# Kernel tuning notes

Hardware: AMD Instinct MI355X
Metric: run time of the kernel (lower is better)

Reference implementation:

```python
import jax, jax.numpy as jnp
import numpy as np

B, L, H, E = 4, 2048, 8, 64

def setup_inputs() -> dict:
    key = jax.random.key(0)
    kq, kk, kv = jax.random.split(key, 3)
    queries = jax.random.normal(kq, (B, L, H, E), dtype=jnp.float32)
    keys = jax.random.normal(kk, (B, L, H, E), dtype=jnp.float32)
    values = jax.random.normal(kv, (B, L, H, E), dtype=jnp.float32)
    return {"queries": queries, "keys": keys, "values": values}

def reference(queries, keys, values):
    # queries/keys/values: [B, L, H, E]
    E_ = queries.shape[-1]
    scale = 1.0 / jnp.sqrt(jnp.float32(E_))
    # scores: [B, H, L, S]
    scores = jnp.einsum('blhe,bshe->bhls', queries, keys)
    Lq, S = scores.shape[-2], scores.shape[-1]
    # TriangularCausalMask: mask positions where s > l (strict upper triangle)
    causal = jnp.tril(jnp.ones((Lq, S), dtype=bool))
    scores = jnp.where(causal, scores, -jnp.inf)
    A = jax.nn.softmax(scale * scores, axis=-1)  # dropout p=0 -> identity
    V = jnp.einsum('bhls,bshd->blhd', A, values)
    return V
```

## Files before the change

kernel.cpp:

```cpp
#include <hip/hip_runtime.h>


#define Bc 4
#define Lc 2048
#define Hc 8
#define Ec 64
#define TILEB 8192
#define NKV 32
#define BHB ((size_t)NKV * TILEB)
#define WSV ((size_t)32 * BHB)

using f32x4 = __attribute__((ext_vector_type(4))) float;
using f16x8 = __attribute__((ext_vector_type(8))) _Float16;
using f16x4 = __attribute__((ext_vector_type(4))) _Float16;
using hf16x2 = __fp16 __attribute__((ext_vector_type(2)));
using u32x4 = __attribute__((ext_vector_type(4))) unsigned int;

static __device__ __forceinline__ unsigned int pk2(float lo, float hi) {
    union { hf16x2 h; unsigned int u; } c;
    c.h = __builtin_amdgcn_cvt_pkrtz(lo, hi);
    return c.u;
}
static __device__ __forceinline__ u32x4 nt16(const void* p) {
    return __builtin_nontemporal_load((const u32x4*)p);
}

__global__ __launch_bounds__(256)
void prep_kernel(const float* __restrict__ K, const float* __restrict__ V,
                 char* __restrict__ ws)
{
    __shared__ char kst[64 * 128];
    __shared__ char vst[64 * 144];
    __shared__ char vtt[64 * 128];

    const int bid = blockIdx.x;
    const int bh = bid >> 5, kt = bid & 31;
    const int b = bh >> 3, h = bh & 7;
    const int tid = threadIdx.x;
    const size_t base = (size_t)b * Lc * Hc * Ec + (size_t)h * Ec;

    {
        const int r = tid >> 2, q4 = tid & 3, c0 = 16 * q4;
        const float* kp = K + base + (size_t)(kt * 64 + r) * 512 + c0;
        const float* vp = V + base + (size_t)(kt * 64 + r) * 512 + c0;
        unsigned int wk[8], wv[8];
        #pragma unroll
        for (int i = 0; i < 4; ++i) {
            union { u32x4 v; float f[4]; } fk, fv;
            fk.v = nt16(kp + 4 * i);
            fv.v = nt16(vp + 4 * i);
            wk[2*i]   = pk2(fk.f[0], fk.f[1]); wk[2*i+1] = pk2(fk.f[2], fk.f[3]);
            wv[2*i]   = pk2(fv.f[0], fv.f[1]); wv[2*i+1] = pk2(fv.f[2], fv.f[3]);
        }
        *(uint4*)(kst + r * 128 + 2 * c0)      = *(uint4*)&wk[0];
        *(uint4*)(kst + r * 128 + 2 * c0 + 16) = *(uint4*)&wk[4];
        *(uint4*)(vst + r * 144 + 2 * c0)      = *(uint4*)&wv[0];
        *(uint4*)(vst + r * 144 + 2 * c0 + 16) = *(uint4*)&wv[4];
    }
    __syncthreads();
    {
        const int e = tid >> 2, kq = tid & 3, kv0 = 16 * kq;
        unsigned int w[8];
        #pragma unroll
        for (int i = 0; i < 8; ++i) {
            unsigned int lo = *(const unsigned short*)(vst + (kv0 + 2*i)     * 144 + 2*e);
            unsigned int hi = *(const unsigned short*)(vst + (kv0 + 2*i + 1) * 144 + 2*e);
            w[i] = lo | (hi << 16);
        }
        *(uint4*)(vtt + e * 128 + 2 * kv0)      = *(uint4*)&w[0];
        *(uint4*)(vtt + e * 128 + 2 * kv0 + 16) = *(uint4*)&w[4];
    }
    __syncthreads();
    {
        const int lane = tid & 63, qq = tid >> 6;
        const int l15 = lane & 15, l4 = lane >> 4;
        char* ko = ws + (size_t)bh * BHB + (size_t)kt * TILEB;
        char* vo = ws + WSV + (size_t)bh * BHB + (size_t)kt * TILEB;
        uint4 k0 = *(const uint4*)(kst + (16 * qq + l15) * 128 + 16 * l4);
        uint4 k1 = *(const uint4*)(kst + (16 * qq + l15) * 128 + 64 + 16 * l4);
        *(uint4*)(ko + (2 * qq)     * 1024 + lane * 16) = k0;
        *(uint4*)(ko + (2 * qq + 1) * 1024 + lane * 16) = k1;
        unsigned long long vv[4];
        #pragma unroll
        for (int c = 0; c < 4; ++c)
            vv[c] = *(const unsigned long long*)(vtt + (16 * c + l15) * 128 + 32 * qq + 8 * l4);
        uint4 v01, v23;
        v01.x = (unsigned)vv[0]; v01.y = (unsigned)(vv[0] >> 32);
        v01.z = (unsigned)vv[1]; v01.w = (unsigned)(vv[1] >> 32);
        v23.x = (unsigned)vv[2]; v23.y = (unsigned)(vv[2] >> 32);
        v23.z = (unsigned)vv[3]; v23.w = (unsigned)(vv[3] >> 32);
        *(uint4*)(vo + (2 * qq)     * 1024 + lane * 16) = v01;
        *(uint4*)(vo + (2 * qq + 1) * 1024 + lane * 16) = v23;
    }
}

__global__ __launch_bounds__(256, 3)
void fa_fwd_kernel(const float* __restrict__ Q, const char* __restrict__ ws,
                   float* __restrict__ Out)
{
    const int bid = blockIdx.x;
    const int qi  = bid >> 5;
    const int bh  = bid & 31;
    const int qt  = 31 - qi;
    const int b   = bh >> 3, h = bh & 7;

    const int tid  = threadIdx.x;
    const int wid  = tid >> 6;
    const int lane = tid & 63;
    const int l15  = lane & 15, l4 = lane >> 4;

    const size_t base = (size_t)b * Lc * Hc * Ec + (size_t)h * Ec;
    const char* kimg = ws + (size_t)bh * BHB + lane * 16;
    const char* vimg = ws + WSV + (size_t)bh * BHB + lane * 16;
    const float SL2E = 0.125f * 1.44269504088896340736f;

    const int qrow0 = qt * 64 + 16 * wid;
    const int mysteps = qt + 1;

    f16x8 qa0, qa1;
    {
        const float* qpr = Q + base + (size_t)(qrow0 + l15) * 512 + 8 * l4;
        union { u32x4 v; float f[4]; } f0, f1, f2, f3;
        f0.v = nt16(qpr);      f1.v = nt16(qpr + 4);
        f2.v = nt16(qpr + 32); f3.v = nt16(qpr + 36);
        union { f16x8 v; unsigned int u[4]; } pk;
        pk.u[0] = pk2(f0.f[0] * SL2E, f0.f[1] * SL2E);
        pk.u[1] = pk2(f0.f[2] * SL2E, f0.f[3] * SL2E);
        pk.u[2] = pk2(f1.f[0] * SL2E, f1.f[1] * SL2E);
        pk.u[3] = pk2(f1.f[2] * SL2E, f1.f[3] * SL2E);
        qa0 = pk.v;
        pk.u[0] = pk2(f2.f[0] * SL2E, f2.f[1] * SL2E);
        pk.u[1] = pk2(f2.f[2] * SL2E, f2.f[3] * SL2E);
        pk.u[2] = pk2(f3.f[0] * SL2E, f3.f[1] * SL2E);
        pk.u[3] = pk2(f3.f[2] * SL2E, f3.f[3] * SL2E);
        qa1 = pk.v;
    }

    f32x4 o[4] = {};
    float lsum = 0.f;
    float m_run = 8.0f;

    uint4 kf[8], vf[8];
    #pragma unroll
    for (int j = 0; j < 8; ++j) kf[j] = *(const uint4*)(kimg + j * 1024);
    #pragma unroll
    for (int j = 0; j < 8; ++j) vf[j] = *(const uint4*)(vimg + j * 1024);

    #pragma unroll 1
    for (int kt = 0; kt < mysteps; ++kt) {
        const int nxt = (kt + 1 < mysteps) ? kt + 1 : kt;
        const char* kp = kimg + (size_t)nxt * TILEB;
        const char* vp = vimg + (size_t)nxt * TILEB;
        const bool last = (kt == mysteps - 1);

        #pragma unroll
        for (int m = 0; m < 4; ++m) {
            union { uint4 u; f16x8 h; } a0, a1;
            a0.u = kf[2 * m]; a1.u = kf[2 * m + 1];
            f32x4 s = {0.f, 0.f, 0.f, 0.f};
            s = __builtin_amdgcn_mfma_f32_16x16x32_f16(a0.h, qa0, s, 0, 0, 0);
            s = __builtin_amdgcn_mfma_f32_16x16x32_f16(a1.h, qa1, s, 0, 0, 0);

            kf[2 * m]     = *(const uint4*)(kp + (2 * m)     * 1024);
            kf[2 * m + 1] = *(const uint4*)(kp + (2 * m + 1) * 1024);

            if (last) {
                const int q_g = qrow0 + l15;
                #pragma unroll
                for (int r2 = 0; r2 < 4; ++r2) {
                    const int kv_g = kt * 64 + 16 * m + 4 * l4 + r2;
                    if (kv_g > q_g) s[r2] = -1e30f;
                }
            }

            const float cmax = fmaxf(fmaxf(s[0], s[1]), fmaxf(s[2], s[3]));
            if (__any(cmax > m_run)) {
                float pm = cmax;
                pm = fmaxf(pm, __shfl_xor(pm, 16, 64));
                pm = fmaxf(pm, __shfl_xor(pm, 32, 64));
                const float m_new = fmaxf(m_run, pm);
                const float fac = __builtin_exp2f(m_run - m_new);
                m_run = m_new;
                lsum *= fac;
                float fr[4];
                #pragma unroll
                for (int r2 = 0; r2 < 4; ++r2) fr[r2] = __shfl(fac, 4 * l4 + r2, 64);
                #pragma unroll
                for (int c = 0; c < 4; ++c)
                    #pragma unroll
                    for (int r2 = 0; r2 < 4; ++r2) o[c][r2] *= fr[r2];
            }

            const float p0 = __builtin_exp2f(s[0] - m_run);
            const float p1 = __builtin_exp2f(s[1] - m_run);
            const float p2 = __builtin_exp2f(s[2] - m_run);
            const float p3 = __builtin_exp2f(s[3] - m_run);
            lsum += (p0 + p1) + (p2 + p3);
            union { f16x4 h; unsigned int u[2]; } pa;
            pa.u[0] = pk2(p0, p1);
            pa.u[1] = pk2(p2, p3);

            union { uint4 u; f16x4 h[2]; } w0, w1;
            w0.u = vf[2 * m]; w1.u = vf[2 * m + 1];
            o[0] = __builtin_amdgcn_mfma_f32_16x16x16f16(pa.h, w0.h[0], o[0], 0, 0, 0);
            o[1] = __builtin_amdgcn_mfma_f32_16x16x16f16(pa.h, w0.h[1], o[1], 0, 0, 0);
            o[2] = __builtin_amdgcn_mfma_f32_16x16x16f16(pa.h, w1.h[0], o[2], 0, 0, 0);
            o[3] = __builtin_amdgcn_mfma_f32_16x16x16f16(pa.h, w1.h[1], o[3], 0, 0, 0);

            vf[2 * m]     = *(const uint4*)(vp + (2 * m)     * 1024);
            vf[2 * m + 1] = *(const uint4*)(vp + (2 * m + 1) * 1024);
        }
    }

    lsum += __shfl_xor(lsum, 16, 64);
    lsum += __shfl_xor(lsum, 32, 64);
    const float inv = 1.0f / lsum;
    float ir[4];
    #pragma unroll
    for (int r2 = 0; r2 < 4; ++r2) ir[r2] = __shfl(inv, 4 * l4 + r2, 64);
    float* op = Out + base;
    #pragma unroll
    for (int c = 0; c < 4; ++c)
        #pragma unroll
        for (int r2 = 0; r2 < 4; ++r2)
            __builtin_nontemporal_store(o[c][r2] * ir[r2],
                op + (size_t)(qrow0 + 4 * l4 + r2) * 512 + 16 * c + l15);
}

extern "C" void kernel_launch(void* const* d_in, const int* in_sizes, int n_in,
                              void* d_out, int out_size, void* d_ws, size_t ws_size,
                              hipStream_t stream) {
    const float* Q = (const float*)d_in[0];
    const float* K = (const float*)d_in[1];
    const float* V = (const float*)d_in[2];
    float* O = (float*)d_out;
    char* ws = (char*)d_ws;
    hipLaunchKernelGGL(prep_kernel, dim3(32 * NKV), dim3(256), 0, stream, K, V, ws);
    hipLaunchKernelGGL(fa_fwd_kernel, dim3(32 * 32), dim3(256), 0, stream, Q, ws, O);
}
```

Before: 67.83 us.

## Process two 16-row query groups per wave to reuse K/V fragments

Each wave now handles 32 query rows (two MFMA groups) and each block handles 128 query rows instead of 64, so every K/V fragment loaded from the workspace feeds two sets of MFMAs. The grid is halved and the q-tile order is changed to a zig-zag over the 16 tiles, with per-wave step counts adjusted for the causal boundary. Occupancy is lowered to 2 blocks per CU because of the extra registers for the doubled accumulators. Waves within a block now have different step counts, and the output stores switch from nontemporal to plain stores.

```diff
diff --git a/kernel.cpp b/kernel.cpp
--- a/kernel.cpp
+++ b/kernel.cpp
@@ -94,14 +94,14 @@
     }
 }
 
-__global__ __launch_bounds__(256, 3)
+__global__ __launch_bounds__(256, 2)
 void fa_fwd_kernel(const float* __restrict__ Q, const char* __restrict__ ws,
                    float* __restrict__ Out)
 {
     const int bid = blockIdx.x;
     const int qi  = bid >> 5;
     const int bh  = bid & 31;
-    const int qt  = 31 - qi;
+    const int qt  = (qi < 8) ? (15 - qi) : (qi - 8);
     const int b   = bh >> 3, h = bh & 7;
 
     const int tid  = threadIdx.x;
@@ -114,12 +114,13 @@
     const char* vimg = ws + WSV + (size_t)bh * BHB + lane * 16;
     const float SL2E = 0.125f * 1.44269504088896340736f;
 
-    const int qrow0 = qt * 64 + 16 * wid;
-    const int mysteps = qt + 1;
-
-    f16x8 qa0, qa1;
-    {
-        const float* qpr = Q + base + (size_t)(qrow0 + l15) * 512 + 8 * l4;
+    const int qrow0 = qt * 128 + 32 * wid;
+    const int mysteps = 2 * qt + 1 + (wid >> 1);
+
+    f16x8 qa[2][2];
+    #pragma unroll
+    for (int g = 0; g < 2; ++g) {
+        const float* qpr = Q + base + (size_t)(qrow0 + 16 * g + l15) * 512 + 8 * l4;
         union { u32x4 v; float f[4]; } f0, f1, f2, f3;
         f0.v = nt16(qpr);      f1.v = nt16(qpr + 4);
         f2.v = nt16(qpr + 32); f3.v = nt16(qpr + 36);
@@ -128,17 +129,17 @@
         pk.u[1] = pk2(f0.f[2] * SL2E, f0.f[3] * SL2E);
         pk.u[2] = pk2(f1.f[0] * SL2E, f1.f[1] * SL2E);
         pk.u[3] = pk2(f1.f[2] * SL2E, f1.f[3] * SL2E);
-        qa0 = pk.v;
+        qa[g][0] = pk.v;
         pk.u[0] = pk2(f2.f[0] * SL2E, f2.f[1] * SL2E);
         pk.u[1] = pk2(f2.f[2] * SL2E, f2.f[3] * SL2E);
         pk.u[2] = pk2(f3.f[0] * SL2E, f3.f[1] * SL2E);
         pk.u[3] = pk2(f3.f[2] * SL2E, f3.f[3] * SL2E);
-        qa1 = pk.v;
-    }
-
-    f32x4 o[4] = {};
-    float lsum = 0.f;
-    float m_run = 8.0f;
+        qa[g][1] = pk.v;
+    }
+
+    f32x4 o[2][4] = {};
+    float lsum[2] = {0.f, 0.f};
+    float m_run[2] = {8.0f, 8.0f};
 
     uint4 kf[8], vf[8];
     #pragma unroll
@@ -148,83 +149,97 @@
 
     #pragma unroll 1
     for (int kt = 0; kt < mysteps; ++kt) {
-        const int nxt = (kt + 1 < mysteps) ? kt + 1 : kt;
-        const char* kp = kimg + (size_t)nxt * TILEB;
-        const char* vp = vimg + (size_t)nxt * TILEB;
         const bool last = (kt == mysteps - 1);
+        const char* kp = kimg + (size_t)(last ? 0 : kt + 1) * TILEB;
+        const char* vp = vimg + (size_t)(last ? 0 : kt + 1) * TILEB;
+        const int kv0 = kt * 64;
 
         #pragma unroll
         for (int m = 0; m < 4; ++m) {
             union { uint4 u; f16x8 h; } a0, a1;
             a0.u = kf[2 * m]; a1.u = kf[2 * m + 1];
-            f32x4 s = {0.f, 0.f, 0.f, 0.f};
-            s = __builtin_amdgcn_mfma_f32_16x16x32_f16(a0.h, qa0, s, 0, 0, 0);
-            s = __builtin_amdgcn_mfma_f32_16x16x32_f16(a1.h, qa1, s, 0, 0, 0);
+            f32x4 s[2];
+            #pragma unroll
+            for (int g = 0; g < 2; ++g) {
+                f32x4 z = {0.f, 0.f, 0.f, 0.f};
+                z = __builtin_amdgcn_mfma_f32_16x16x32_f16(a0.h, qa[g][0], z, 0, 0, 0);
+                z = __builtin_amdgcn_mfma_f32_16x16x32_f16(a1.h, qa[g][1], z, 0, 0, 0);
+                s[g] = z;
+            }
 
             kf[2 * m]     = *(const uint4*)(kp + (2 * m)     * 1024);
             kf[2 * m + 1] = *(const uint4*)(kp + (2 * m + 1) * 1024);
 
             if (last) {
-                const int q_g = qrow0 + l15;
                 #pragma unroll
-                for (int r2 = 0; r2 < 4; ++r2) {
-                    const int kv_g = kt * 64 + 16 * m + 4 * l4 + r2;
-                    if (kv_g > q_g) s[r2] = -1e30f;
+                for (int g = 0; g < 2; ++g) {
+                    const int q_g = qrow0 + 16 * g + l15;
+                    #pragma unroll
+                    for (int r2 = 0; r2 < 4; ++r2) {
+                        const int kv_g = kv0 + 16 * m + 4 * l4 + r2;
+                        if (kv_g > q_g) s[g][r2] = -1e30f;
+                    }
                 }
             }
 
-            const float cmax = fmaxf(fmaxf(s[0], s[1]), fmaxf(s[2], s[3]));
-            if (__any(cmax > m_run)) {
-                float pm = cmax;
-                pm = fmaxf(pm, __shfl_xor(pm, 16, 64));
-                pm = fmaxf(pm, __shfl_xor(pm, 32, 64));
-                const float m_new = fmaxf(m_run, pm);
-                const float fac = __builtin_exp2f(m_run - m_new);
-                m_run = m_new;
-                lsum *= fac;
-                float fr[4];
-                #pragma unroll
-                for (int r2 = 0; r2 < 4; ++r2) fr[r2] = __shfl(fac, 4 * l4 + r2, 64);
-                #pragma unroll
-                for (int c = 0; c < 4; ++c)
-                    #pragma unroll
-                    for (int r2 = 0; r2 < 4; ++r2) o[c][r2] *= fr[r2];
-            }
-
-            const float p0 = __builtin_exp2f(s[0] - m_run);
-            const float p1 = __builtin_exp2f(s[1] - m_run);
-            const float p2 = __builtin_exp2f(s[2] - m_run);
-            const float p3 = __builtin_exp2f(s[3] - m_run);
-            lsum += (p0 + p1) + (p2 + p3);
-            union { f16x4 h; unsigned int u[2]; } pa;
-            pa.u[0] = pk2(p0, p1);
-            pa.u[1] = pk2(p2, p3);
-
             union { uint4 u; f16x4 h[2]; } w0, w1;
             w0.u = vf[2 * m]; w1.u = vf[2 * m + 1];
-            o[0] = __builtin_amdgcn_mfma_f32_16x16x16f16(pa.h, w0.h[0], o[0], 0, 0, 0);
-            o[1] = __builtin_amdgcn_mfma_f32_16x16x16f16(pa.h, w0.h[1], o[1], 0, 0, 0);
-            o[2] = __builtin_amdgcn_mfma_f32_16x16x16f16(pa.h, w1.h[0], o[2], 0, 0, 0);
-            o[3] = __builtin_amdgcn_mfma_f32_16x16x16f16(pa.h, w1.h[1], o[3], 0, 0, 0);
+            #pragma unroll
+            for (int g = 0; g < 2; ++g) {
+                const float cmax = fmaxf(fmaxf(s[g][0], s[g][1]),
+                                         fmaxf(s[g][2], s[g][3]));
+                if (__any(cmax > m_run[g])) {
+                    float pm = cmax;
+                    pm = fmaxf(pm, __shfl_xor(pm, 16, 64));
+                    pm = fmaxf(pm, __shfl_xor(pm, 32, 64));
+                    const float m_new = fmaxf(m_run[g], pm);
+                    const float fac = __builtin_exp2f(m_run[g] - m_new);
+                    m_run[g] = m_new;
+                    lsum[g] *= fac;
+                    float fr[4];
+                    #pragma unroll
+                    for (int r2 = 0; r2 < 4; ++r2) fr[r2] = __shfl(fac, 4 * l4 + r2, 64);
+                    #pragma unroll
+                    for (int c = 0; c < 4; ++c)
+                        #pragma unroll
+                        for (int r2 = 0; r2 < 4; ++r2) o[g][c][r2] *= fr[r2];
+                }
+                const float p0 = __builtin_exp2f(s[g][0] - m_run[g]);
+                const float p1 = __builtin_exp2f(s[g][1] - m_run[g]);
+                const float p2 = __builtin_exp2f(s[g][2] - m_run[g]);
+                const float p3 = __builtin_exp2f(s[g][3] - m_run[g]);
+                lsum[g] += (p0 + p1) + (p2 + p3);
+                union { f16x4 h; unsigned int u[2]; } pa;
+                pa.u[0] = pk2(p0, p1);
+                pa.u[1] = pk2(p2, p3);
+                o[g][0] = __builtin_amdgcn_mfma_f32_16x16x16f16(pa.h, w0.h[0], o[g][0], 0, 0, 0);
+                o[g][1] = __builtin_amdgcn_mfma_f32_16x16x16f16(pa.h, w0.h[1], o[g][1], 0, 0, 0);
+                o[g][2] = __builtin_amdgcn_mfma_f32_16x16x16f16(pa.h, w1.h[0], o[g][2], 0, 0, 0);
+                o[g][3] = __builtin_amdgcn_mfma_f32_16x16x16f16(pa.h, w1.h[1], o[g][3], 0, 0, 0);
+            }
 
             vf[2 * m]     = *(const uint4*)(vp + (2 * m)     * 1024);
             vf[2 * m + 1] = *(const uint4*)(vp + (2 * m + 1) * 1024);
         }
     }
 
-    lsum += __shfl_xor(lsum, 16, 64);
-    lsum += __shfl_xor(lsum, 32, 64);
-    const float inv = 1.0f / lsum;
-    float ir[4];
-    #pragma unroll
-    for (int r2 = 0; r2 < 4; ++r2) ir[r2] = __shfl(inv, 4 * l4 + r2, 64);
     float* op = Out + base;
     #pragma unroll
-    for (int c = 0; c < 4; ++c)
-        #pragma unroll
-        for (int r2 = 0; r2 < 4; ++r2)
-            __builtin_nontemporal_store(o[c][r2] * ir[r2],
-                op + (size_t)(qrow0 + 4 * l4 + r2) * 512 + 16 * c + l15);
+    for (int g = 0; g < 2; ++g) {
+        float ls = lsum[g];
+        ls += __shfl_xor(ls, 16, 64);
+        ls += __shfl_xor(ls, 32, 64);
+        const float inv = 1.0f / ls;
+        float ir[4];
+        #pragma unroll
+        for (int r2 = 0; r2 < 4; ++r2) ir[r2] = __shfl(inv, 4 * l4 + r2, 64);
+        const int qr = qrow0 + 16 * g;
+        #pragma unroll
+        for (int c = 0; c < 4; ++c)
+            #pragma unroll
+            for (int r2 = 0; r2 < 4; ++r2)
+                op[(size_t)(qr + 4 * l4 + r2) * 512 + 16 * c + l15] = o[g][c][r2] * ir[r2];
+    }
 }
 
 extern "C" void kernel_launch(void* const* d_in, const int* in_sizes, int n_in,
@@ -236,5 +251,5 @@
     float* O = (float*)d_out;
     char* ws = (char*)d_ws;
     hipLaunchKernelGGL(prep_kernel, dim3(32 * NKV), dim3(256), 0, stream, K, V, ws);
-    hipLaunchKernelGGL(fa_fwd_kernel, dim3(32 * 32), dim3(256), 0, stream, Q, ws, O);
-}
+    hipLaunchKernelGGL(fa_fwd_kernel, dim3(16 * 32), dim3(256), 0, stream, Q, ws, O);
+}
```

New measurement: 69.37 us. 1.02x slower.

## Split long causal query tiles across two KV-halves with a merge kernel

Applied to the files above, without the earlier changes.

The 16 longest query tiles per head now have their KV loop split into two halves run by separate blocks. Each half writes unnormalized output, row sum and running max to a workspace slot, and a new merge kernel combines them with log-sum-exp weights. This balances the triangular causal workload and shortens the critical path of the longest blocks. Launch bounds also rise to 4 blocks per CU. The cost is an extra kernel launch and the partial-result traffic through the workspace, and the path falls back to the old kernel if the workspace is too small.

```diff
diff --git a/kernel.cpp b/kernel.cpp
--- a/kernel.cpp
+++ b/kernel.cpp
@@ -9,6 +9,8 @@
 #define NKV 32
 #define BHB ((size_t)NKV * TILEB)
 #define WSV ((size_t)32 * BHB)
+#define WSP ((size_t)64 * BHB)
+#define SLOT 17408
 
 using f32x4 = __attribute__((ext_vector_type(4))) float;
 using f16x8 = __attribute__((ext_vector_type(8))) _Float16;
@@ -94,15 +96,35 @@
     }
 }
 
-__global__ __launch_bounds__(256, 3)
-void fa_fwd_kernel(const float* __restrict__ Q, const char* __restrict__ ws,
+template<bool SPLIT>
+__global__ __launch_bounds__(256, 4)
+void fa_fwd_kernel(const float* __restrict__ Q, char* __restrict__ ws,
                    float* __restrict__ Out)
 {
     const int bid = blockIdx.x;
-    const int qi  = bid >> 5;
-    const int bh  = bid & 31;
-    const int qt  = 31 - qi;
-    const int b   = bh >> 3, h = bh & 7;
+    int qt, bh, kt0, kt1;
+    bool wpart = false;
+    char* slotp = nullptr;
+    if (SPLIT) {
+        if (bid < 1024) {
+            const int sq = bid >> 6; qt = 31 - sq;
+            const int rem = bid & 63;
+            const int half = rem >> 5; bh = rem & 31;
+            const int n0 = (qt + 2) >> 1;
+            kt0 = half ? n0 : 0;
+            kt1 = half ? (qt + 1) : n0;
+            wpart = true;
+            slotp = ws + WSP + (size_t)((sq << 6) + (bh << 1) + half) * SLOT;
+        } else {
+            const int u = bid - 1024;
+            qt = 15 - (u >> 5); bh = u & 31;
+            kt0 = 0; kt1 = qt + 1;
+        }
+    } else {
+        qt = 31 - (bid >> 5); bh = bid & 31;
+        kt0 = 0; kt1 = qt + 1;
+    }
+    const int b = bh >> 3, h = bh & 7;
 
     const int tid  = threadIdx.x;
     const int wid  = tid >> 6;
@@ -115,11 +137,11 @@
     const float SL2E = 0.125f * 1.44269504088896340736f;
 
     const int qrow0 = qt * 64 + 16 * wid;
-    const int mysteps = qt + 1;
+    const int q_g = qrow0 + l15;
 
     f16x8 qa0, qa1;
     {
-        const float* qpr = Q + base + (size_t)(qrow0 + l15) * 512 + 8 * l4;
+        const float* qpr = Q + base + (size_t)q_g * 512 + 8 * l4;
         union { u32x4 v; float f[4]; } f0, f1, f2, f3;
         f0.v = nt16(qpr);      f1.v = nt16(qpr + 4);
         f2.v = nt16(qpr + 32); f3.v = nt16(qpr + 36);
@@ -142,16 +164,16 @@
 
     uint4 kf[8], vf[8];
     #pragma unroll
-    for (int j = 0; j < 8; ++j) kf[j] = *(const uint4*)(kimg + j * 1024);
+    for (int j = 0; j < 8; ++j) kf[j] = *(const uint4*)(kimg + (size_t)kt0 * TILEB + j * 1024);
     #pragma unroll
-    for (int j = 0; j < 8; ++j) vf[j] = *(const uint4*)(vimg + j * 1024);
+    for (int j = 0; j < 8; ++j) vf[j] = *(const uint4*)(vimg + (size_t)kt0 * TILEB + j * 1024);
 
     #pragma unroll 1
-    for (int kt = 0; kt < mysteps; ++kt) {
-        const int nxt = (kt + 1 < mysteps) ? kt + 1 : kt;
+    for (int kt = kt0; kt < kt1; ++kt) {
+        const bool last = (kt == qt);
+        const int nxt = (kt + 1 < kt1) ? kt + 1 : kt0;
         const char* kp = kimg + (size_t)nxt * TILEB;
         const char* vp = vimg + (size_t)nxt * TILEB;
-        const bool last = (kt == mysteps - 1);
 
         #pragma unroll
         for (int m = 0; m < 4; ++m) {
@@ -165,7 +187,6 @@
             kf[2 * m + 1] = *(const uint4*)(kp + (2 * m + 1) * 1024);
 
             if (last) {
-                const int q_g = qrow0 + l15;
                 #pragma unroll
                 for (int r2 = 0; r2 < 4; ++r2) {
                     const int kv_g = kt * 64 + 16 * m + 4 * l4 + r2;
@@ -214,17 +235,70 @@
 
     lsum += __shfl_xor(lsum, 16, 64);
     lsum += __shfl_xor(lsum, 32, 64);
-    const float inv = 1.0f / lsum;
-    float ir[4];
+
+    if (SPLIT && wpart) {
+        float* po = (float*)slotp;
+        #pragma unroll
+        for (int c = 0; c < 4; ++c)
+            #pragma unroll
+            for (int r2 = 0; r2 < 4; ++r2)
+                po[(16 * wid + 4 * l4 + r2) * 64 + 16 * c + l15] = o[c][r2];
+        if (l4 == 0) {
+            ((float*)(slotp + 16384))[16 * wid + l15] = lsum;
+            ((float*)(slotp + 16640))[16 * wid + l15] = m_run;
+        }
+    } else {
+        const float inv = 1.0f / lsum;
+        float ir[4];
+        #pragma unroll
+        for (int r2 = 0; r2 < 4; ++r2) ir[r2] = __shfl(inv, 4 * l4 + r2, 64);
+        float* op = Out + base;
+        #pragma unroll
+        for (int c = 0; c < 4; ++c)
+            #pragma unroll
+            for (int r2 = 0; r2 < 4; ++r2)
+                op[(size_t)(qrow0 + 4 * l4 + r2) * 512 + 16 * c + l15] = o[c][r2] * ir[r2];
+    }
+}
+
+__global__ __launch_bounds__(256)
+void merge_kernel(const char* __restrict__ ws, float* __restrict__ Out)
+{
+    const int bid = blockIdx.x;
+    const int sq = bid >> 5;
+    const int qt = 31 - sq;
+    const int bh = bid & 31;
+    const int b = bh >> 3, h = bh & 7;
+    const char* s0 = ws + WSP + (size_t)((sq << 6) + (bh << 1)) * SLOT;
+    const char* s1 = s0 + SLOT;
+
+    const int tid = threadIdx.x;
+    const int row = tid >> 2, cq = tid & 3;
+
+    const float l0 = ((const float*)(s0 + 16384))[row];
+    const float l1 = ((const float*)(s1 + 16384))[row];
+    const float m0 = ((const float*)(s0 + 16640))[row];
+    const float m1 = ((const float*)(s1 + 16640))[row];
+    const float ms = fmaxf(m0, m1);
+    const float w0 = __builtin_exp2f(m0 - ms);
+    const float w1 = __builtin_exp2f(m1 - ms);
+    const float inv = 1.0f / (l0 * w0 + l1 * w1);
+
+    const float* o0 = (const float*)s0 + row * 64 + 16 * cq;
+    const float* o1 = (const float*)s1 + row * 64 + 16 * cq;
+    float* op = Out + (size_t)b * Lc * Hc * Ec + (size_t)h * Ec
+              + (size_t)(qt * 64 + row) * 512 + 16 * cq;
     #pragma unroll
-    for (int r2 = 0; r2 < 4; ++r2) ir[r2] = __shfl(inv, 4 * l4 + r2, 64);
-    float* op = Out + base;
-    #pragma unroll
-    for (int c = 0; c < 4; ++c)
-        #pragma unroll
-        for (int r2 = 0; r2 < 4; ++r2)
-            __builtin_nontemporal_store(o[c][r2] * ir[r2],
-                op + (size_t)(qrow0 + 4 * l4 + r2) * 512 + 16 * c + l15);
+    for (int i = 0; i < 4; ++i) {
+        float4 a = *(const float4*)(o0 + 4 * i);
+        float4 c = *(const float4*)(o1 + 4 * i);
+        float4 r;
+        r.x = (a.x * w0 + c.x * w1) * inv;
+        r.y = (a.y * w0 + c.y * w1) * inv;
+        r.z = (a.z * w0 + c.z * w1) * inv;
+        r.w = (a.w * w0 + c.w * w1) * inv;
+        *(float4*)(op + 4 * i) = r;
+    }
 }
 
 extern "C" void kernel_launch(void* const* d_in, const int* in_sizes, int n_in,
@@ -235,6 +309,12 @@
     const float* V = (const float*)d_in[2];
     float* O = (float*)d_out;
     char* ws = (char*)d_ws;
-    hipLaunchKernelGGL(prep_kernel, dim3(32 * NKV), dim3(256), 0, stream, K, V, ws);
-    hipLaunchKernelGGL(fa_fwd_kernel, dim3(32 * 32), dim3(256), 0, stream, Q, ws, O);
-}
+    const size_t NEED = WSP + (size_t)1024 * SLOT;
+    prep_kernel<<<dim3(32 * NKV), dim3(256), 0, stream>>>(K, V, ws);
+    if (ws_size >= NEED) {
+        fa_fwd_kernel<true><<<dim3(1536), dim3(256), 0, stream>>>(Q, ws, O);
+        merge_kernel<<<dim3(512), dim3(256), 0, stream>>>(ws, O);
+    } else {
+        fa_fwd_kernel<false><<<dim3(1024), dim3(256), 0, stream>>>(Q, ws, O);
+    }
+}
```

Result: slower. 71.68 us (+5.7%).
